# Performance work log

Measured on AMD Instinct MI355X. Metric: run time of the kernel, lower is better.

The kernel has to match this reference:

```python
import jax, jax.numpy as jnp
import numpy as np
import math

B, S, D, H, MLP, L = 4, 1024, 512, 8, 2048, 4
C = D // H  # head dim = 64
K_RATIO = 0.25
TOPK = max(1, min(S, int(math.ceil(K_RATIO * S))))  # 256
EPS = 1e-6


def layernorm(x, w, b):
    mu = jnp.mean(x, axis=-1, keepdims=True)
    var = jnp.mean(jnp.square(x - mu), axis=-1, keepdims=True)
    return (x - mu) * jax.lax.rsqrt(var + EPS) * w + b


def dwconv3(x, w):
    # x: (B, Ch, S), w: (Ch, 1, 3) depthwise conv, padding 1
    return jax.lax.conv_general_dilated(
        x, w, window_strides=(1,), padding=[(1, 1)],
        dimension_numbers=('NCH', 'OIH', 'NCH'),
        feature_group_count=x.shape[1])


def setup_inputs() -> dict:
    key = jax.random.key(0)
    ks = jax.random.split(key, 16)
    g = lambda k, shape, s=0.02: jax.random.normal(k, shape, jnp.float32) * s
    return {
        'x': jax.random.normal(ks[0], (B, S, D), jnp.float32),
        'pos_emb': g(ks[1], (1, S, D)),
        'ln1_w': jnp.ones((L, D), jnp.float32),
        'ln1_b': jnp.zeros((L, D), jnp.float32),
        'qkv_w': g(ks[2], (L, 3 * D, D)),
        'dw_w': g(ks[3], (L, 3 * D, 1, 3), 0.1),
        'temp': jnp.ones((L, H), jnp.float32),
        'proj_w': g(ks[4], (L, D, D)),
        'ln2_w': jnp.ones((L, D), jnp.float32),
        'ln2_b': jnp.zeros((L, D), jnp.float32),
        'mlp_w1': g(ks[5], (L, MLP, D)),
        'mlp_b1': g(ks[6], (L, MLP), 1e-6),
        'mlp_w2': g(ks[7], (L, D, MLP)),
        'mlp_b2': g(ks[8], (L, D), 1e-6),
        'lnf_w': jnp.ones((D,), jnp.float32),
        'lnf_b': jnp.zeros((D,), jnp.float32),
    }


def _block(x, ln1_w, ln1_b, qkv_w, dw_w, temp, proj_w, ln2_w, ln2_b,
           mlp_w1, mlp_b1, mlp_w2, mlp_b2):
    # x: (B, S, D)
    h = layernorm(x, ln1_w, ln1_b).swapaxes(1, 2)        # (B, D, S)
    qkv = jnp.einsum('od,bds->bos', qkv_w, h)            # (B, 3D, S) 1x1 conv
    qkv = dwconv3(qkv, dw_w)                             # depthwise k=3
    q, k, v = jnp.split(qkv, 3, axis=1)                  # each (B, D, S)
    # 'b (head c) s -> b head s c'
    to_heads = lambda t: t.reshape(B, H, C, S).transpose(0, 1, 3, 2)
    q, k, v = to_heads(q), to_heads(k), to_heads(v)      # (B, H, S, C)
    q = q / jnp.maximum(jnp.linalg.norm(q, axis=-1, keepdims=True), 1e-12)
    k = k / jnp.maximum(jnp.linalg.norm(k, axis=-1, keepdims=True), 1e-12)
    scores = jnp.einsum('bhsc,bhtc->bhst', q, k) * temp[None, :, None, None]
    # top-k per query row: keep entries >= k-th largest, mask rest to -inf
    kth = jax.lax.top_k(scores, TOPK)[0][..., -1:]       # (B, H, S, 1)
    sparse = jnp.where(scores >= kth, scores, -jnp.inf)
    sparse = jnp.clip(sparse, -10000.0, 10000.0)         # -inf -> -10000
    attn = jax.nn.softmax(sparse, axis=-1)
    out = jnp.einsum('bhst,bhtc->bhsc', attn, v)         # (B, H, S, C)
    out = out.transpose(0, 1, 3, 2).reshape(B, D, S)     # 'b head s c -> b (head c) s'
    out = jnp.einsum('od,bds->bos', proj_w, out)         # project_out 1x1 conv
    x = x + out.swapaxes(1, 2)                           # residual (dropout=0)
    y = layernorm(x, ln2_w, ln2_b)
    y = jax.nn.gelu(y @ mlp_w1.T + mlp_b1, approximate=False) @ mlp_w2.T + mlp_b2
    return x + y


def reference(x, pos_emb, ln1_w, ln1_b, qkv_w, dw_w, temp, proj_w,
              ln2_w, ln2_b, mlp_w1, mlp_b1, mlp_w2, mlp_b2, lnf_w, lnf_b):
    h = x + pos_emb
    for i in range(L):
        h = _block(h, ln1_w[i], ln1_b[i], qkv_w[i], dw_w[i], temp[i], proj_w[i],
                   ln2_w[i], ln2_b[i], mlp_w1[i], mlp_b1[i], mlp_w2[i], mlp_b2[i])
    return layernorm(h, lnf_w, lnf_b)
```

## Files before the change

kernel.cpp:

```cpp
#include <hip/hip_runtime.h>

#define NB   4
#define SEQ  1024
#define DIM  512
#define NH   8
#define HD   64
#define MLPD 2048
#define NL   4
#define TOPKK 256
#define QKVD 1536
#define QT   16

typedef short bh8 __attribute__((ext_vector_type(8)));
typedef float f32x4 __attribute__((ext_vector_type(4)));

__device__ __forceinline__ float b2f(unsigned short v) {
    return __uint_as_float(((unsigned)v) << 16);
}
__device__ __forceinline__ unsigned short f2b(float f) {
    unsigned u = __float_as_uint(f);
    u += 0x7FFFu + ((u >> 16) & 1u);
    return (unsigned short)(u >> 16);
}
__device__ __forceinline__ float ldin(const void* p, size_t i, int bf) {
    return bf ? b2f(((const unsigned short*)p)[i]) : ((const float*)p)[i];
}
__device__ __forceinline__ float wave_sum(float v) {
#pragma unroll
    for (int m = 32; m; m >>= 1) v += __shfl_xor(v, m);
    return v;
}
__device__ __forceinline__ unsigned f2key16(unsigned short u) {
    return (u & 0x8000u) ? (unsigned)((~u) & 0xFFFFu) : (unsigned)(u | 0x8000u);
}
__device__ __forceinline__ unsigned short key16b(unsigned k) {
    return (k & 0x8000u) ? (unsigned short)(k & 0x7FFFu)
                         : (unsigned short)((~k) & 0xFFFFu);
}
__device__ __forceinline__ unsigned cvtpk(float a, float b) {
    unsigned r;
    asm("v_cvt_pk_bf16_f32 %0, %1, %2" : "=v"(r) : "v"(a), "v"(b));
    return r;
}
__device__ __forceinline__ uint4 pack8(const float* __restrict__ p) {
    uint4 r;
    r.x = (unsigned)f2b(p[0]) | ((unsigned)f2b(p[1]) << 16);
    r.y = (unsigned)f2b(p[2]) | ((unsigned)f2b(p[3]) << 16);
    r.z = (unsigned)f2b(p[4]) | ((unsigned)f2b(p[5]) << 16);
    r.w = (unsigned)f2b(p[6]) | ((unsigned)f2b(p[7]) << 16);
    return r;
}
__device__ __forceinline__ void async16(unsigned short* lds, const unsigned short* g) {
    __builtin_amdgcn_global_load_lds(
        (const __attribute__((address_space(1))) unsigned int*)g,
        (__attribute__((address_space(3))) unsigned int*)lds, 16, 0, 0);
}


__global__ void detect_kernel(const unsigned short* __restrict__ ln1w,
                              int* __restrict__ flag) {
    if (threadIdx.x == 0 && blockIdx.x == 0)
        *flag = (ln1w[0] == 0x3F80u) ? 1 : 0;
}

__global__ __launch_bounds__(256) void wcvt_kernel(
    const void* __restrict__ W, unsigned short* __restrict__ out,
    int n, const int* __restrict__ dflag) {
    int bf = *dflag;
    int idx = blockIdx.x * 256 + threadIdx.x;
    if (idx < n) out[idx] = f2b(ldin(W, idx, bf));
}

__global__ __launch_bounds__(256) void addpos_kernel(
    const void* __restrict__ x, const void* __restrict__ pos,
    float* __restrict__ h, const int* __restrict__ dflag) {
    int bf = *dflag;
    int idx = blockIdx.x * 256 + threadIdx.x;
    int sd = idx & (SEQ * DIM - 1);
    h[idx] = ldin(x, idx, bf) + ldin(pos, sd, bf);
}

__global__ __launch_bounds__(256) void ln_kernel(
    const float* __restrict__ in, const void* __restrict__ w,
    const void* __restrict__ bb, size_t wo, unsigned short* __restrict__ out,
    const int* __restrict__ dflag) {
    int bf = *dflag;
    int tid = threadIdx.x;
    int lane = tid & 63, wid = tid >> 6;
    int row = blockIdx.x * 4 + wid;
    const float* p = in + (size_t)row * DIM + lane * 8;
    float4 x0 = *(const float4*)(p);
    float4 x1 = *(const float4*)(p + 4);
    float d[8] = {x0.x, x0.y, x0.z, x0.w, x1.x, x1.y, x1.z, x1.w};
    float s = (d[0] + d[1]) + (d[2] + d[3]) + (d[4] + d[5]) + (d[6] + d[7]);
    s = wave_sum(s);
    float mean = s * (1.0f / DIM);
    float q = 0.f;
#pragma unroll
    for (int j = 0; j < 8; ++j) {
        d[j] -= mean;
        q += d[j] * d[j];
    }
    q = wave_sum(q);
    float rs = rsqrtf(q * (1.0f / DIM) + 1e-6f);
    size_t eo = wo + lane * 8;
    unsigned short* o = out + (size_t)row * DIM + lane * 8;
    unsigned pw[4];
#pragma unroll
    for (int j = 0; j < 4; ++j) {
        float v0 = d[2 * j]     * rs * ldin(w, eo + 2 * j, bf)     + ldin(bb, eo + 2 * j, bf);
        float v1 = d[2 * j + 1] * rs * ldin(w, eo + 2 * j + 1, bf) + ldin(bb, eo + 2 * j + 1, bf);
        pw[j] = (unsigned)f2b(v0) | ((unsigned)f2b(v1) << 16);
    }
    *(uint4*)o = (uint4){pw[0], pw[1], pw[2], pw[3]};
}

__global__ __launch_bounds__(256) void lnf_kernel(
    const float* __restrict__ in, const void* __restrict__ w,
    const void* __restrict__ bb, void* __restrict__ out,
    const int* __restrict__ dflag) {
    int bf = *dflag;
    __shared__ float red[4];
    int row = blockIdx.x, tid = threadIdx.x;
    int lane = tid & 63, wid = tid >> 6;
    const float* p = in + (size_t)row * DIM;
    float x0 = p[tid], x1 = p[tid + 256];
    float s = wave_sum(x0 + x1);
    if (!lane) red[wid] = s;
    __syncthreads();
    float mean = (red[0] + red[1] + red[2] + red[3]) * (1.0f / DIM);
    float d0 = x0 - mean, d1 = x1 - mean;
    float q = wave_sum(d0 * d0 + d1 * d1);
    __syncthreads();
    if (!lane) red[wid] = q;
    __syncthreads();
    float var = (red[0] + red[1] + red[2] + red[3]) * (1.0f / DIM);
    float rs = rsqrtf(var + 1e-6f);
    float v0 = d0 * rs * ldin(w, tid, bf) + ldin(bb, tid, bf);
    float v1 = d1 * rs * ldin(w, tid + 256, bf) + ldin(bb, tid + 256, bf);
    size_t o = (size_t)row * DIM;
    if (bf) {
        ((unsigned short*)out)[o + tid]       = f2b(v0);
        ((unsigned short*)out)[o + tid + 256] = f2b(v1);
    } else {
        ((float*)out)[o + tid]       = v0;
        ((float*)out)[o + tid + 256] = v1;
    }
}

__global__ __launch_bounds__(256) void gemm_mfma_kernel(
    const unsigned short* __restrict__ A, const void* __restrict__ W, size_t wo,
    const void* __restrict__ bias, size_t bo, void* __restrict__ C,
    int M, int N, int K, int flags, const int* __restrict__ dflag) {
    int bf = *dflag;
    __shared__ unsigned short As[128 * 32];
    __shared__ unsigned short Bs[128 * 32];
    int tid = threadIdx.x;
    int w = tid >> 6, l = tid & 63;
    int n0 = blockIdx.x * 128, m0 = blockIdx.y * 128;
    int wm = (w >> 1) * 64, wn = (w & 1) * 64;
    int lq = l & 15, lk = l >> 4;

    int srow = w * 32 + (l >> 2);
    int cb = (l & 3) * 8;
    const unsigned short* aG = A + (size_t)(m0 + srow) * K + cb;
    size_t wb = wo + (size_t)(n0 + srow) * K + cb;
    unsigned short* sA0 = &As[w * 1024 + l * 8];
    unsigned short* sA1 = &As[w * 1024 + 512 + l * 8];
    unsigned short* sB0 = &Bs[w * 1024 + l * 8];
    unsigned short* sB1 = &Bs[w * 1024 + 512 + l * 8];

    f32x4 acc[4][4];
#pragma unroll
    for (int i = 0; i < 4; ++i)
#pragma unroll
        for (int j = 0; j < 4; ++j)
            acc[i][j] = (f32x4){0.f, 0.f, 0.f, 0.f};

    for (int k0 = 0; k0 < K; k0 += 32) {
        uint4 a0 = *(const uint4*)(aG + k0);
        uint4 a1 = *(const uint4*)(aG + 16 * K + k0);
        uint4 b0, b1;
        if (bf) {
            b0 = *(const uint4*)((const unsigned short*)W + wb + k0);
            b1 = *(const uint4*)((const unsigned short*)W + wb + 16 * K + k0);
        } else {
            b0 = pack8((const float*)W + wb + k0);
            b1 = pack8((const float*)W + wb + 16 * K + k0);
        }
        __syncthreads();
        *(uint4*)sA0 = a0;
        *(uint4*)sA1 = a1;
        *(uint4*)sB0 = b0;
        *(uint4*)sB1 = b1;
        __syncthreads();
        bh8 af[4], bw[4];
#pragma unroll
        for (int i = 0; i < 4; ++i) {
            af[i] = *(const bh8*)&As[(wm + i * 16 + lq) * 32 + lk * 8];
            bw[i] = *(const bh8*)&Bs[(wn + i * 16 + lq) * 32 + lk * 8];
        }
#pragma unroll
        for (int i = 0; i < 4; ++i)
#pragma unroll
            for (int j = 0; j < 4; ++j)
                acc[i][j] = __builtin_amdgcn_mfma_f32_16x16x32_bf16(
                    af[i], bw[j], acc[i][j], 0, 0, 0);
    }

    int lr4 = lk * 4;
#pragma unroll
    for (int i = 0; i < 4; ++i) {
#pragma unroll
        for (int j = 0; j < 4; ++j) {
            int n = n0 + wn + j * 16 + lq;
            float bv = (flags & 4) ? ldin(bias, bo + n, bf) : 0.0f;
#pragma unroll
            for (int r = 0; r < 4; ++r) {
                int m = m0 + wm + i * 16 + lr4 + r;
                float v = acc[i][j][r] + bv;
                if (flags & 2) v = 0.5f * v * (1.0f + erff(v * 0.70710678118654752f));
                size_t o = (size_t)m * N + n;
                if (flags & 1) ((float*)C)[o] += v;
                else           ((unsigned short*)C)[o] = f2b(v);
            }
        }
    }
}

__global__ __launch_bounds__(256) void gemm_mfma_n64_kernel(
    const unsigned short* __restrict__ A, const void* __restrict__ W, size_t wo,
    const void* __restrict__ bias, size_t bo, void* __restrict__ C,
    int M, int N, int K, int flags, const int* __restrict__ dflag) {
    int bf = *dflag;
    __shared__ unsigned short As[128 * 32];
    __shared__ unsigned short Bs[64 * 32];
    int tid = threadIdx.x;
    int w = tid >> 6, l = tid & 63;
    int n0 = blockIdx.x * 64, m0 = blockIdx.y * 128;
    int wm = (w >> 1) * 64, wn = (w & 1) * 32;
    int lq = l & 15, lk = l >> 4;

    int srowA = w * 32 + (l >> 2);
    int cb = (l & 3) * 8;
    const unsigned short* aG = A + (size_t)(m0 + srowA) * K + cb;
    int srowB = w * 16 + (l >> 2);
    size_t wb = wo + (size_t)(n0 + srowB) * K + cb;
    unsigned short* sA0 = &As[w * 1024 + l * 8];
    unsigned short* sA1 = &As[w * 1024 + 512 + l * 8];
    unsigned short* sB0 = &Bs[w * 512 + l * 8];

    f32x4 acc[4][2];
#pragma unroll
    for (int i = 0; i < 4; ++i) {
        acc[i][0] = (f32x4){0.f, 0.f, 0.f, 0.f};
        acc[i][1] = (f32x4){0.f, 0.f, 0.f, 0.f};
    }

    for (int k0 = 0; k0 < K; k0 += 32) {
        uint4 a0 = *(const uint4*)(aG + k0);
        uint4 a1 = *(const uint4*)(aG + 16 * K + k0);
        uint4 b0;
        if (bf) b0 = *(const uint4*)((const unsigned short*)W + wb + k0);
        else    b0 = pack8((const float*)W + wb + k0);
        __syncthreads();
        *(uint4*)sA0 = a0;
        *(uint4*)sA1 = a1;
        *(uint4*)sB0 = b0;
        __syncthreads();
        bh8 af[4], bw[2];
#pragma unroll
        for (int i = 0; i < 4; ++i)
            af[i] = *(const bh8*)&As[(wm + i * 16 + lq) * 32 + lk * 8];
        bw[0] = *(const bh8*)&Bs[(wn + lq) * 32 + lk * 8];
        bw[1] = *(const bh8*)&Bs[(wn + 16 + lq) * 32 + lk * 8];
#pragma unroll
        for (int i = 0; i < 4; ++i) {
            acc[i][0] = __builtin_amdgcn_mfma_f32_16x16x32_bf16(af[i], bw[0], acc[i][0], 0, 0, 0);
            acc[i][1] = __builtin_amdgcn_mfma_f32_16x16x32_bf16(af[i], bw[1], acc[i][1], 0, 0, 0);
        }
    }

    int lr4 = lk * 4;
#pragma unroll
    for (int i = 0; i < 4; ++i) {
#pragma unroll
        for (int j = 0; j < 2; ++j) {
            int n = n0 + wn + j * 16 + lq;
            float bv = (flags & 4) ? ldin(bias, bo + n, bf) : 0.0f;
#pragma unroll
            for (int r = 0; r < 4; ++r) {
                int m = m0 + wm + i * 16 + lr4 + r;
                float v = acc[i][j][r] + bv;
                if (flags & 2) v = 0.5f * v * (1.0f + erff(v * 0.70710678118654752f));
                size_t o = (size_t)m * N + n;
                if (flags & 1) ((float*)C)[o] += v;
                else           ((unsigned short*)C)[o] = f2b(v);
            }
        }
    }
}

__global__ __launch_bounds__(256) void gemm_n64_dlds_kernel(
    const unsigned short* __restrict__ A, const unsigned short* __restrict__ W, size_t wo,
    const void* __restrict__ bias, size_t bo, void* __restrict__ C,
    int M, int N, int K, int flags, const int* __restrict__ dflag) {
    __shared__ unsigned short As[2][128 * 32];
    __shared__ unsigned short Bs[2][64 * 32];
    int tid = threadIdx.x;
    int w = tid >> 6, l = tid & 63;
    int n0 = blockIdx.x * 64, m0 = blockIdx.y * 128;
    int kz = blockIdx.z;
    int Ks = K / (int)gridDim.z;
    int kbeg = kz * Ks;
    int nt = Ks / 32;
    int wm = (w >> 1) * 64, wn = (w & 1) * 32;
    int lq = l & 15, lk = l >> 4;

    int srowA = w * 32 + (l >> 2);
    int srowB = w * 16 + (l >> 2);
    int cb = (l & 3) * 8;
    const unsigned short* aG = A + (size_t)(m0 + srowA) * K + cb + kbeg;
    const unsigned short* wG = W + wo + (size_t)(n0 + srowB) * K + cb + kbeg;

    f32x4 acc[4][2];
#pragma unroll
    for (int i = 0; i < 4; ++i) {
        acc[i][0] = (f32x4){0.f, 0.f, 0.f, 0.f};
        acc[i][1] = (f32x4){0.f, 0.f, 0.f, 0.f};
    }

    async16(&As[0][w * 1024], aG);
    async16(&As[0][w * 1024 + 512], aG + 16 * K);
    async16(&Bs[0][w * 512], wG);

    int cur = 0;
    for (int t = 0; t < nt; ++t) {
        asm volatile("s_waitcnt vmcnt(0)" ::: "memory");
        __builtin_amdgcn_s_barrier();
        if (t + 1 < nt) {
            int k1 = (t + 1) * 32;
            async16(&As[cur ^ 1][w * 1024], aG + k1);
            async16(&As[cur ^ 1][w * 1024 + 512], aG + 16 * K + k1);
            async16(&Bs[cur ^ 1][w * 512], wG + k1);
        }
        bh8 af[4], bw[2];
#pragma unroll
        for (int i = 0; i < 4; ++i)
            af[i] = *(const bh8*)&As[cur][(wm + i * 16 + lq) * 32 + lk * 8];
        bw[0] = *(const bh8*)&Bs[cur][(wn + lq) * 32 + lk * 8];
        bw[1] = *(const bh8*)&Bs[cur][(wn + 16 + lq) * 32 + lk * 8];
#pragma unroll
        for (int i = 0; i < 4; ++i) {
            acc[i][0] = __builtin_amdgcn_mfma_f32_16x16x32_bf16(af[i], bw[0], acc[i][0], 0, 0, 0);
            acc[i][1] = __builtin_amdgcn_mfma_f32_16x16x32_bf16(af[i], bw[1], acc[i][1], 0, 0, 0);
        }
        cur ^= 1;
    }

    int bf = (flags & 4) ? *dflag : 0;
    int lr4 = lk * 4;
#pragma unroll
    for (int i = 0; i < 4; ++i) {
#pragma unroll
        for (int j = 0; j < 2; ++j) {
            int n = n0 + wn + j * 16 + lq;
            float bv = ((flags & 4) && kz == 0) ? ldin(bias, bo + n, bf) : 0.0f;
#pragma unroll
            for (int r = 0; r < 4; ++r) {
                int m = m0 + wm + i * 16 + lr4 + r;
                float v = acc[i][j][r] + bv;
                if (flags & 2) v = 0.5f * v * (1.0f + erff(v * 0.70710678118654752f));
                size_t o = (size_t)m * N + n;
                if (flags & 8)      atomicAdd(&((float*)C)[o], v);
                else if (flags & 1) ((float*)C)[o] += v;
                else                ((unsigned short*)C)[o] = f2b(v);
            }
        }
    }
}

__global__ __launch_bounds__(256) void dwqkv_kernel(
    const unsigned short* __restrict__ in, const void* __restrict__ w, size_t wo,
    const void* __restrict__ temp, size_t to,
    unsigned short* __restrict__ qn, unsigned short* __restrict__ Kc,
    unsigned short* __restrict__ Vt, const int* __restrict__ dflag) {
    int bf = *dflag;
    int tid = threadIdx.x;
    int g = tid >> 6, c = tid & 63;
    int gid = blockIdx.x * 4 + g;
    int h = gid & 7;
    int bs = gid >> 3;
    int s = bs & (SEQ - 1), b = bs >> 10;
    int bh = b * NH + h;
    const unsigned short* row = in + (size_t)bs * QKVD;
    float vals[3];
#pragma unroll
    for (int t = 0; t < 3; ++t) {
        int o = t * 512 + h * HD + c;
        float w0 = ldin(w, wo + o * 3 + 0, bf);
        float w1 = ldin(w, wo + o * 3 + 1, bf);
        float w2 = ldin(w, wo + o * 3 + 2, bf);
        float a = w1 * b2f(row[o]);
        if (s > 0)       a += w0 * b2f(row[o - QKVD]);
        if (s < SEQ - 1) a += w2 * b2f(row[o + QKVD]);
        vals[t] = a;
    }
    float qs = wave_sum(vals[0] * vals[0]);
    float ks = wave_sum(vals[1] * vals[1]);
    float t_ = ldin(temp, to + h, bf);
    qn[(size_t)bs * DIM + h * HD + c] = f2b(vals[0] / fmaxf(sqrtf(qs), 1e-12f) * t_);
    Kc[((size_t)bh * SEQ + s) * HD + c] = f2b(vals[1] / fmaxf(sqrtf(ks), 1e-12f));
    Vt[(((size_t)bh * 32 + (s >> 5)) * HD + c) * 32 + (s & 31)] = f2b(vals[2]);
}

__global__ __launch_bounds__(256) void attn_kernel(
    const unsigned short* __restrict__ q, const unsigned short* __restrict__ Kc,
    const unsigned short* __restrict__ Vt, unsigned short* __restrict__ outp) {
    __shared__ __align__(16) unsigned short sc16[QT * 1024];

    int tid = threadIdx.x;
    int w = tid >> 6, l = tid & 63;
    int lq = l & 15, lk = l >> 4;
    int bid = blockIdx.x;
    int qt = (bid >> 3) & 63;
    int bh = ((bid >> 9) << 3) | (bid & 7);
    int h = bh & 7;
    int b = bh >> 3;

    const unsigned short* qp = q + (size_t)(b * SEQ + qt * QT + lq) * DIM + h * HD + lk * 8;
    bh8 aq0 = *(const bh8*)(qp);
    bh8 aq1 = *(const bh8*)(qp + 32);

    int swz = ((lq ^ (lq >> 2)) & 7) << 1;

    const unsigned short* Kbh = Kc + (size_t)bh * SEQ * HD;
    unsigned short* srowq = sc16 + lq * 1024;
    for (int kb = 0; kb < 16; kb += 2) {
        int key0 = (w * 16 + kb) * 16;
        const unsigned short* kp0 = Kbh + (size_t)(key0 + lq) * HD + lk * 8;
        const unsigned short* kp1 = kp0 + 16 * HD;
        bh8 b0 = *(const bh8*)(kp0);
        bh8 b1 = *(const bh8*)(kp0 + 32);
        bh8 b2 = *(const bh8*)(kp1);
        bh8 b3 = *(const bh8*)(kp1 + 32);
        f32x4 a0 = {0.f, 0.f, 0.f, 0.f};
        f32x4 a1 = {0.f, 0.f, 0.f, 0.f};
        a0 = __builtin_amdgcn_mfma_f32_16x16x32_bf16(b0, aq0, a0, 0, 0, 0);
        a0 = __builtin_amdgcn_mfma_f32_16x16x32_bf16(b1, aq1, a0, 0, 0, 0);
        a1 = __builtin_amdgcn_mfma_f32_16x16x32_bf16(b2, aq0, a1, 0, 0, 0);
        a1 = __builtin_amdgcn_mfma_f32_16x16x32_bf16(b3, aq1, a1, 0, 0, 0);
        int c0 = (key0 >> 2) + lk;
        uint2 w0 = {cvtpk(a0[0], a0[1]), cvtpk(a0[2], a0[3])};
        uint2 w1 = {cvtpk(a1[0], a1[1]), cvtpk(a1[2], a1[3])};
        *(uint2*)&srowq[(c0 ^ swz) << 2]       = w0;
        *(uint2*)&srowq[((c0 + 4) ^ swz) << 2] = w1;
    }
    __syncthreads();

    for (int rr = 0; rr < 4; rr += 2) {
        int rowA = w * 4 + rr;
        unsigned short* sAr = sc16 + rowA * 1024;
        unsigned short* sBr = sc16 + (rowA + 1) * 1024;
        uint4 ra0 = *(const uint4*)&sAr[l * 8];
        uint4 ra1 = *(const uint4*)&sAr[512 + l * 8];
        uint4 rb0 = *(const uint4*)&sBr[l * 8];
        uint4 rb1 = *(const uint4*)&sBr[512 + l * 8];
        unsigned wa[8] = {ra0.x, ra0.y, ra0.z, ra0.w, ra1.x, ra1.y, ra1.z, ra1.w};
        unsigned wb[8] = {rb0.x, rb0.y, rb0.z, rb0.w, rb1.x, rb1.y, rb1.z, rb1.w};
        float va[16], vb[16];
#pragma unroll
        for (int j = 0; j < 8; ++j) {
            va[2 * j]     = __uint_as_float(wa[j] << 16);
            va[2 * j + 1] = __uint_as_float(wa[j] & 0xFFFF0000u);
            vb[2 * j]     = __uint_as_float(wb[j] << 16);
            vb[2 * j + 1] = __uint_as_float(wb[j] & 0xFFFF0000u);
        }
        float ma = va[0], mb = vb[0];
#pragma unroll
        for (int j = 1; j < 16; ++j) {
            ma = fmaxf(ma, va[j]);
            mb = fmaxf(mb, vb[j]);
        }
#pragma unroll
        for (int off = 1; off < 64; off <<= 1) {
            ma = fmaxf(ma, __shfl_xor(ma, off));
            mb = fmaxf(mb, __shfl_xor(mb, off));
        }
        ma = fminf(fmaxf(ma, -10000.f), 10000.f);
        mb = fminf(fmaxf(mb, -10000.f), 10000.f);
        unsigned Ta = 0, Tb = 0;
        for (int bit = 15; bit >= 0; --bit) {
            unsigned ca = Ta | (1u << bit), cb = Tb | (1u << bit);
            float tfa = b2f(key16b(ca)), tfb = b2f(key16b(cb));
            unsigned cna = 0, cnb = 0;
#pragma unroll
            for (int j = 0; j < 16; ++j) {
                cna += (unsigned)__popcll(__ballot(va[j] >= tfa));
                cnb += (unsigned)__popcll(__ballot(vb[j] >= tfb));
            }
            if (cna >= TOPKK) Ta = ca;
            if (cnb >= TOPKK) Tb = cb;
        }
        float ka = b2f(key16b(Ta)), kb = b2f(key16b(Tb));
        float sa = 0.f, sb = 0.f;
#pragma unroll
        for (int j = 0; j < 16; ++j) {
            float aa = fminf(fmaxf(va[j], -10000.f), 10000.f);
            float ab = fminf(fmaxf(vb[j], -10000.f), 10000.f);
            float ea = (va[j] >= ka) ? __expf(aa - ma) : 0.0f;
            float eb = (vb[j] >= kb) ? __expf(ab - mb) : 0.0f;
            sa += ea; sb += eb;
            va[j] = ea; vb[j] = eb;
        }
#pragma unroll
        for (int off = 1; off < 64; off <<= 1) {
            sa += __shfl_xor(sa, off);
            sb += __shfl_xor(sb, off);
        }
        float ia = 1.0f / sa, ib = 1.0f / sb;
        unsigned pa[8], pb[8];
#pragma unroll
        for (int j = 0; j < 8; ++j) {
            pa[j] = cvtpk(va[2 * j] * ia, va[2 * j + 1] * ia);
            pb[j] = cvtpk(vb[2 * j] * ib, vb[2 * j + 1] * ib);
        }
        *(uint4*)&sAr[l * 8]       = (uint4){pa[0], pa[1], pa[2], pa[3]};
        *(uint4*)&sAr[512 + l * 8] = (uint4){pa[4], pa[5], pa[6], pa[7]};
        *(uint4*)&sBr[l * 8]       = (uint4){pb[0], pb[1], pb[2], pb[3]};
        *(uint4*)&sBr[512 + l * 8] = (uint4){pb[4], pb[5], pb[6], pb[7]};
    }
    __syncthreads();

    {
        const unsigned short* Vbh = Vt + (size_t)bh * SEQ * HD;
        const unsigned short* prow = sc16 + lq * 1024;
        f32x4 oacc = {0.f, 0.f, 0.f, 0.f};
        for (int tc = 0; tc < 32; tc += 2) {
            const unsigned short* vp0 = Vbh + (size_t)tc * 2048 + (w * 16 + lq) * 32 + lk * 8;
            bh8 bv0 = *(const bh8*)(vp0);
            bh8 bv1 = *(const bh8*)(vp0 + 2048);
            bh8 ap0 = *(const bh8*)&prow[((tc * 8 + lk * 2) ^ swz) << 2];
            bh8 ap1 = *(const bh8*)&prow[(((tc + 1) * 8 + lk * 2) ^ swz) << 2];
            oacc = __builtin_amdgcn_mfma_f32_16x16x32_bf16(ap0, bv0, oacc, 0, 0, 0);
            oacc = __builtin_amdgcn_mfma_f32_16x16x32_bf16(ap1, bv1, oacc, 0, 0, 0);
        }
#pragma unroll
        for (int r = 0; r < 4; ++r) {
            int qrow = lk * 4 + r;
            outp[((size_t)(b * SEQ + qt * QT + qrow)) * DIM + h * HD + w * 16 + lq] = f2b(oacc[r]);
        }
    }
}

extern "C" void kernel_launch(void* const* d_in, const int* in_sizes, int n_in,
                              void* d_out, int out_size, void* d_ws, size_t ws_size,
                              hipStream_t stream) {
    (void)in_sizes; (void)n_in; (void)out_size;
    const void* x     = d_in[0];
    const void* pos   = d_in[1];
    const void* ln1w  = d_in[2];
    const void* ln1b  = d_in[3];
    const void* qkvw  = d_in[4];
    const void* dww   = d_in[5];
    const void* temp  = d_in[6];
    const void* projw = d_in[7];
    const void* ln2w  = d_in[8];
    const void* ln2b  = d_in[9];
    const void* w1    = d_in[10];
    const void* b1    = d_in[11];
    const void* w2    = d_in[12];
    const void* b2    = d_in[13];
    const void* lnfw  = d_in[14];
    const void* lnfb  = d_in[15];

    float* wsf = (float*)d_ws;
    const size_t M1 = (size_t)1024 * 1024;
    float*          h    = wsf;
    unsigned short* bn   = (unsigned short*)(wsf + 2 * M1);
    unsigned short* C2   = (unsigned short*)(wsf + 3 * M1);
    unsigned short* Vt   = (unsigned short*)(wsf + 6 * M1);
    unsigned short* Kc   = (unsigned short*)(wsf + 7 * M1);
    unsigned short* Mb   = C2;
    int*            flag = (int*)(wsf + 9 * M1);
    unsigned short* Wc   = (unsigned short*)(wsf + 9 * M1 + 16);

    const int MTOK  = NB * SEQ;
    const int nQKVW = NL * QKVD * DIM;
    const int nPROJ = NL * DIM * DIM;
    const int nW1   = NL * MLPD * DIM;
    const int nW2   = NL * DIM * MLPD;
    const size_t wcElems = (size_t)nQKVW + nPROJ + nW1 + nW2;
    const int big = ws_size >= ((9 * M1 + 16) * 4 + wcElems * 2);

    unsigned short* WcQ  = Wc;
    unsigned short* WcP  = Wc + nQKVW;
    unsigned short* WcW1 = Wc + nQKVW + nPROJ;
    unsigned short* WcW2 = Wc + nQKVW + nPROJ + (size_t)nW1;

    detect_kernel<<<1, 64, 0, stream>>>((const unsigned short*)ln1w, flag);
    addpos_kernel<<<(NB * SEQ * DIM) / 256, 256, 0, stream>>>(x, pos, h, flag);

    if (big) {
        wcvt_kernel<<<nQKVW / 256, 256, 0, stream>>>(qkvw, WcQ, nQKVW, flag);
        wcvt_kernel<<<nPROJ / 256, 256, 0, stream>>>(projw, WcP, nPROJ, flag);
        wcvt_kernel<<<nW1 / 256, 256, 0, stream>>>(w1, WcW1, nW1, flag);
        wcvt_kernel<<<nW2 / 256, 256, 0, stream>>>(w2, WcW2, nW2, flag);
    }

    for (int l = 0; l < NL; ++l) {
        ln_kernel<<<MTOK / 4, 256, 0, stream>>>(h, ln1w, ln1b, (size_t)l * DIM, bn, flag);
        if (big) {
            gemm_n64_dlds_kernel<<<dim3(QKVD / 64, MTOK / 128, 1), 256, 0, stream>>>(
                bn, WcQ, (size_t)l * QKVD * DIM, nullptr, 0, C2,
                MTOK, QKVD, DIM, 0, flag);
        } else {
            gemm_mfma_kernel<<<dim3(QKVD / 128, MTOK / 128), 256, 0, stream>>>(
                bn, qkvw, (size_t)l * QKVD * DIM, nullptr, 0, C2,
                MTOK, QKVD, DIM, 0, flag);
        }
        dwqkv_kernel<<<(NB * SEQ * NH) / 4, 256, 0, stream>>>(
            C2, dww, (size_t)l * QKVD * 3, temp, (size_t)l * NH, bn, Kc, Vt, flag);
        attn_kernel<<<NB * NH * (SEQ / QT), 256, 0, stream>>>(bn, Kc, Vt, bn);
        if (big) {
            gemm_n64_dlds_kernel<<<dim3(DIM / 64, MTOK / 128, 2), 256, 0, stream>>>(
                bn, WcP, (size_t)l * DIM * DIM, nullptr, 0, h,
                MTOK, DIM, DIM, 8, flag);
        } else {
            gemm_mfma_n64_kernel<<<dim3(DIM / 64, MTOK / 128), 256, 0, stream>>>(
                bn, projw, (size_t)l * DIM * DIM, nullptr, 0, h,
                MTOK, DIM, DIM, 1, flag);
        }
        ln_kernel<<<MTOK / 4, 256, 0, stream>>>(h, ln2w, ln2b, (size_t)l * DIM, bn, flag);
        if (big) {
            gemm_n64_dlds_kernel<<<dim3(MLPD / 64, MTOK / 128, 1), 256, 0, stream>>>(
                bn, WcW1, (size_t)l * MLPD * DIM, b1, (size_t)l * MLPD, Mb,
                MTOK, MLPD, DIM, 2 | 4, flag);
            gemm_n64_dlds_kernel<<<dim3(DIM / 64, MTOK / 128, 2), 256, 0, stream>>>(
                Mb, WcW2, (size_t)l * DIM * MLPD, b2, (size_t)l * DIM, h,
                MTOK, DIM, MLPD, 8 | 4, flag);
        } else {
            gemm_mfma_kernel<<<dim3(MLPD / 128, MTOK / 128), 256, 0, stream>>>(
                bn, w1, (size_t)l * MLPD * DIM, b1, (size_t)l * MLPD, Mb,
                MTOK, MLPD, DIM, 2 | 4, flag);
            gemm_mfma_n64_kernel<<<dim3(DIM / 64, MTOK / 128), 256, 0, stream>>>(
                Mb, w2, (size_t)l * DIM * MLPD, b2, (size_t)l * DIM, h,
                MTOK, DIM, MLPD, 1 | 4, flag);
        }
    }

    lnf_kernel<<<MTOK, 256, 0, stream>>>(h, lnfw, lnfb, d_out, flag);
}
```

Before: 1.010 ms.

## Replace split-K atomics with partial buffer reduced in following layernorm

The split-K projection and MLP-down GEMMs no longer use float atomicAdd into the residual. The first K-slice adds into h directly and the second writes a separate partial buffer. The next layernorm (or the final layernorm) adds that partial, writes the summed residual back, and normalizes. This removes atomic traffic and contention, at the cost of an extra fp32 read in the layernorm kernels and reuse of workspace regions as partial buffers.

```diff
diff --git a/kernel.cpp b/kernel.cpp
--- a/kernel.cpp
+++ b/kernel.cpp
@@ -81,17 +81,26 @@
 }
 
 __global__ __launch_bounds__(256) void ln_kernel(
-    const float* __restrict__ in, const void* __restrict__ w,
-    const void* __restrict__ bb, size_t wo, unsigned short* __restrict__ out,
-    const int* __restrict__ dflag) {
+    float* __restrict__ io, const float* __restrict__ P,
+    const void* __restrict__ w, const void* __restrict__ bb, size_t wo,
+    unsigned short* __restrict__ out, const int* __restrict__ dflag) {
     int bf = *dflag;
     int tid = threadIdx.x;
     int lane = tid & 63, wid = tid >> 6;
     int row = blockIdx.x * 4 + wid;
-    const float* p = in + (size_t)row * DIM + lane * 8;
+    float* p = io + (size_t)row * DIM + lane * 8;
     float4 x0 = *(const float4*)(p);
     float4 x1 = *(const float4*)(p + 4);
     float d[8] = {x0.x, x0.y, x0.z, x0.w, x1.x, x1.y, x1.z, x1.w};
+    if (P) {
+        const float* pp = P + (size_t)row * DIM + lane * 8;
+        float4 q0 = *(const float4*)(pp);
+        float4 q1 = *(const float4*)(pp + 4);
+        d[0] += q0.x; d[1] += q0.y; d[2] += q0.z; d[3] += q0.w;
+        d[4] += q1.x; d[5] += q1.y; d[6] += q1.z; d[7] += q1.w;
+        *(float4*)(p)     = (float4){d[0], d[1], d[2], d[3]};
+        *(float4*)(p + 4) = (float4){d[4], d[5], d[6], d[7]};
+    }
     float s = (d[0] + d[1]) + (d[2] + d[3]) + (d[4] + d[5]) + (d[6] + d[7]);
     s = wave_sum(s);
     float mean = s * (1.0f / DIM);
@@ -116,15 +125,20 @@
 }
 
 __global__ __launch_bounds__(256) void lnf_kernel(
-    const float* __restrict__ in, const void* __restrict__ w,
-    const void* __restrict__ bb, void* __restrict__ out,
-    const int* __restrict__ dflag) {
+    const float* __restrict__ in, const float* __restrict__ P,
+    const void* __restrict__ w, const void* __restrict__ bb,
+    void* __restrict__ out, const int* __restrict__ dflag) {
     int bf = *dflag;
     __shared__ float red[4];
     int row = blockIdx.x, tid = threadIdx.x;
     int lane = tid & 63, wid = tid >> 6;
     const float* p = in + (size_t)row * DIM;
     float x0 = p[tid], x1 = p[tid + 256];
+    if (P) {
+        const float* pp = P + (size_t)row * DIM;
+        x0 += pp[tid];
+        x1 += pp[tid + 256];
+    }
     float s = wave_sum(x0 + x1);
     if (!lane) red[wid] = s;
     __syncthreads();
@@ -304,6 +318,7 @@
 __global__ __launch_bounds__(256) void gemm_n64_dlds_kernel(
     const unsigned short* __restrict__ A, const unsigned short* __restrict__ W, size_t wo,
     const void* __restrict__ bias, size_t bo, void* __restrict__ C,
+    float* __restrict__ Cp,
     int M, int N, int K, int flags, const int* __restrict__ dflag) {
     __shared__ unsigned short As[2][128 * 32];
     __shared__ unsigned short Bs[2][64 * 32];
@@ -372,9 +387,11 @@
                 float v = acc[i][j][r] + bv;
                 if (flags & 2) v = 0.5f * v * (1.0f + erff(v * 0.70710678118654752f));
                 size_t o = (size_t)m * N + n;
-                if (flags & 8)      atomicAdd(&((float*)C)[o], v);
-                else if (flags & 1) ((float*)C)[o] += v;
-                else                ((unsigned short*)C)[o] = f2b(v);
+                if (flags & 8) {
+                    if (kz == 0) ((float*)C)[o] += v;
+                    else         Cp[o] = v;
+                } else if (flags & 1) ((float*)C)[o] += v;
+                else                  ((unsigned short*)C)[o] = f2b(v);
             }
         }
     }
@@ -582,6 +599,8 @@
     unsigned short* Vt   = (unsigned short*)(wsf + 6 * M1);
     unsigned short* Kc   = (unsigned short*)(wsf + 7 * M1);
     unsigned short* Mb   = C2;
+    float*          Pp   = wsf + 3 * M1;
+    float*          Pm   = wsf + 7 * M1;
     int*            flag = (int*)(wsf + 9 * M1);
     unsigned short* Wc   = (unsigned short*)(wsf + 9 * M1 + 16);
 
@@ -609,10 +628,11 @@
     }
 
     for (int l = 0; l < NL; ++l) {
-        ln_kernel<<<MTOK / 4, 256, 0, stream>>>(h, ln1w, ln1b, (size_t)l * DIM, bn, flag);
+        const float* P1 = (big && l > 0) ? Pm : nullptr;
+        ln_kernel<<<MTOK / 4, 256, 0, stream>>>(h, P1, ln1w, ln1b, (size_t)l * DIM, bn, flag);
         if (big) {
             gemm_n64_dlds_kernel<<<dim3(QKVD / 64, MTOK / 128, 1), 256, 0, stream>>>(
-                bn, WcQ, (size_t)l * QKVD * DIM, nullptr, 0, C2,
+                bn, WcQ, (size_t)l * QKVD * DIM, nullptr, 0, C2, nullptr,
                 MTOK, QKVD, DIM, 0, flag);
         } else {
             gemm_mfma_kernel<<<dim3(QKVD / 128, MTOK / 128), 256, 0, stream>>>(
@@ -624,20 +644,21 @@
         attn_kernel<<<NB * NH * (SEQ / QT), 256, 0, stream>>>(bn, Kc, Vt, bn);
         if (big) {
             gemm_n64_dlds_kernel<<<dim3(DIM / 64, MTOK / 128, 2), 256, 0, stream>>>(
-                bn, WcP, (size_t)l * DIM * DIM, nullptr, 0, h,
+                bn, WcP, (size_t)l * DIM * DIM, nullptr, 0, h, Pp,
                 MTOK, DIM, DIM, 8, flag);
         } else {
             gemm_mfma_n64_kernel<<<dim3(DIM / 64, MTOK / 128), 256, 0, stream>>>(
                 bn, projw, (size_t)l * DIM * DIM, nullptr, 0, h,
                 MTOK, DIM, DIM, 1, flag);
         }
-        ln_kernel<<<MTOK / 4, 256, 0, stream>>>(h, ln2w, ln2b, (size_t)l * DIM, bn, flag);
+        ln_kernel<<<MTOK / 4, 256, 0, stream>>>(h, big ? Pp : nullptr,
+                                                ln2w, ln2b, (size_t)l * DIM, bn, flag);
         if (big) {
             gemm_n64_dlds_kernel<<<dim3(MLPD / 64, MTOK / 128, 1), 256, 0, stream>>>(
-                bn, WcW1, (size_t)l * MLPD * DIM, b1, (size_t)l * MLPD, Mb,
+                bn, WcW1, (size_t)l * MLPD * DIM, b1, (size_t)l * MLPD, Mb, nullptr,
                 MTOK, MLPD, DIM, 2 | 4, flag);
             gemm_n64_dlds_kernel<<<dim3(DIM / 64, MTOK / 128, 2), 256, 0, stream>>>(
-                Mb, WcW2, (size_t)l * DIM * MLPD, b2, (size_t)l * DIM, h,
+                Mb, WcW2, (size_t)l * DIM * MLPD, b2, (size_t)l * DIM, h, Pm,
                 MTOK, DIM, MLPD, 8 | 4, flag);
         } else {
             gemm_mfma_kernel<<<dim3(MLPD / 128, MTOK / 128), 256, 0, stream>>>(
@@ -649,5 +670,5 @@
         }
     }
 
-    lnf_kernel<<<MTOK, 256, 0, stream>>>(h, lnfw, lnfb, d_out, flag);
-}
+    lnf_kernel<<<MTOK, 256, 0, stream>>>(h, big ? Pm : nullptr, lnfw, lnfb, d_out, flag);
+}
```

Result: slower. 1.031 ms (+2.1%).
